# Kernel tuning notes

Measured on AMD Instinct MI355X. Metric: run time of the kernel, lower is better.

Reference implementation:

```python
import jax, jax.numpy as jnp
import numpy as np

H = 4       # N_head
C = 32      # c_hidden
CZ = 128    # c_z
N = 256
B = 1
EPS = 1e-5


def setup_inputs() -> dict:
    key = jax.random.key(0)
    ks = jax.random.split(key, 8)
    hc = H * C
    return {
        "z": jax.random.normal(ks[0], (B, N, N, CZ), dtype=jnp.float32),
        "ln_scale": jnp.ones((CZ,), dtype=jnp.float32),
        "ln_bias": jnp.zeros((CZ,), dtype=jnp.float32),
        "Wq": jax.random.normal(ks[1], (CZ, hc), dtype=jnp.float32) * 0.02,
        "Wk": jax.random.normal(ks[2], (CZ, hc), dtype=jnp.float32) * 0.02,
        "Wv": jax.random.normal(ks[3], (CZ, hc), dtype=jnp.float32) * 0.02,
        "Wb": jax.random.normal(ks[4], (CZ, H), dtype=jnp.float32) * 0.02,
        "Wg": jax.random.normal(ks[5], (CZ, hc), dtype=jnp.float32) * 0.02,
        "Wo": jax.random.normal(ks[6], (hc, CZ), dtype=jnp.float32) * 0.02,
    }


def reference(z, ln_scale, ln_bias, Wq, Wk, Wv, Wb, Wg, Wo):
    b, n = z.shape[0], z.shape[1]
    # LayerNorm over c_z
    mu = jnp.mean(z, axis=-1, keepdims=True)
    var = jnp.mean(jnp.square(z - mu), axis=-1, keepdims=True)
    zn = (z - mu) * jax.lax.rsqrt(var + EPS) * ln_scale + ln_bias
    # projections -> [B, N, N, H, C]
    q = (zn @ Wq).reshape(b, n, n, H, C)
    k = (zn @ Wk).reshape(b, n, n, H, C)
    v = (zn @ Wv).reshape(b, n, n, H, C)
    bias = zn @ Wb                                  # [B, N, N, H]
    g = jax.nn.sigmoid(zn @ Wg).reshape(b, n, n, H, C)
    # attention around starting node i: query at (i,j), keys/values at (i,k)
    scores = jnp.einsum('bijhd,bikhd->bijkh', q, k) * (1.0 / C ** 0.5)
    scores = scores + bias[:, None, :, :, :]        # bias[b, j, k, h]
    a = jax.nn.softmax(scores, axis=-2)             # softmax over k
    o = jnp.einsum('bijkh,bikhd->bijhd', a, v)      # [B, N, N, H, C]
    o = (g * o).reshape(b, n, n, H * C)
    return o @ Wo
```

## Files before the change

### kernel.cpp

```cpp
#include <hip/hip_runtime.h>
#include <math.h>

#define NN 256
#define CZ 128
#define NH 4
#define CH 32
#define HC 128
#define NPIX (NN*NN)
#define L2E   1.4426950408889634f
#define SCALE2 (0.17677669529663687f * 1.4426950408889634f)

typedef __attribute__((ext_vector_type(8))) short bf16x8;
typedef __attribute__((ext_vector_type(4))) float fx4;
typedef __attribute__((ext_vector_type(4))) unsigned u32x4;

__device__ __forceinline__ unsigned pack_hl(float x) {
    unsigned b  = __builtin_bit_cast(unsigned, x);
    unsigned hb = b & 0xFFFF0000u;
    float r = x - __builtin_bit_cast(float, hb);
    return hb | (__builtin_bit_cast(unsigned, r) >> 16);
}
__device__ __forceinline__ void load_split8(const float* p, bf16x8& h, bf16x8& l) {
    float4 x0 = *(const float4*)p;
    float4 x1 = *(const float4*)(p + 4);
    float xs[8] = {x0.x, x0.y, x0.z, x0.w, x1.x, x1.y, x1.z, x1.w};
    #pragma unroll
    for (int j = 0; j < 8; ++j) {
        unsigned b  = __builtin_bit_cast(unsigned, xs[j]);
        unsigned hb = b & 0xFFFF0000u;
        float r = xs[j] - __builtin_bit_cast(float, hb);
        h[j] = (short)(hb >> 16);
        l[j] = (short)(__builtin_bit_cast(unsigned, r) >> 16);
    }
}
__device__ __forceinline__ void deint8(const unsigned* p, bf16x8& h, bf16x8& l) {
    u32x4 e0 = *(const u32x4*)p;
    u32x4 e1 = *(const u32x4*)(p + 4);
    unsigned es[8] = {e0[0], e0[1], e0[2], e0[3], e1[0], e1[1], e1[2], e1[3]};
    unsigned hw[4], lw[4];
    #pragma unroll
    for (int j = 0; j < 4; ++j) {
        unsigned a = es[2 * j], b = es[2 * j + 1];
        hw[j] = (a >> 16) | (b & 0xFFFF0000u);
        lw[j] = (a & 0x0000FFFFu) | (b << 16);
    }
    h = __builtin_bit_cast(bf16x8, u32x4{hw[0], hw[1], hw[2], hw[3]});
    l = __builtin_bit_cast(bf16x8, u32x4{lw[0], lw[1], lw[2], lw[3]});
}

__global__ __launch_bounds__(256) void pack_w_kernel(
    const float* __restrict__ Wq, const float* __restrict__ Wk,
    const float* __restrict__ Wv, const float* __restrict__ Wg,
    const float* __restrict__ Wo, bf16x8* __restrict__ pk)
{
    int id  = blockIdx.x * 256 + threadIdx.x;
    int mid = id >> 11;
    int e   = id & 2047;
    const float* W = (mid == 0) ? Wq : (mid == 1) ? Wk : (mid == 2) ? Wv : (mid == 3) ? Wg : Wo;
    int quad = e & 3, n = (e >> 2) & 127, ks = e >> 9;
    int k0 = ks * 32 + quad * 8;
    bf16x8 h, l;
    #pragma unroll
    for (int j = 0; j < 8; ++j) {
        float x = W[(size_t)(k0 + j) * 128 + n];
        unsigned b  = __builtin_bit_cast(unsigned, x);
        unsigned hb = b & 0xFFFF0000u;
        float r = x - __builtin_bit_cast(float, hb);
        h[j] = (short)(hb >> 16);
        l[j] = (short)(__builtin_bit_cast(unsigned, r) >> 16);
    }
    pk[(size_t)mid * 4096 + e]        = h;
    pk[(size_t)mid * 4096 + 2048 + e] = l;
}

__global__ __launch_bounds__(256) void ln_proj_kernel(
    const float* __restrict__ z, const float* __restrict__ ls, const float* __restrict__ lb,
    const float* __restrict__ Wb, const bf16x8* __restrict__ pk,
    unsigned* __restrict__ q_pk, unsigned* __restrict__ k_pk, unsigned* __restrict__ v_pk,
    float* __restrict__ g_ws, float* __restrict__ bias_n)
{
    __shared__ float zsh[32][132];
    __shared__ float rsum[256], rsq[256];
    __shared__ float pmu[32], prs[32];

    const int t  = threadIdx.x;
    const int p0 = blockIdx.x * 32;
    const int i  = p0 >> 8;
    const int j0 = p0 & 255;

    const float4* z4 = (const float4*)(z + (size_t)p0 * CZ);
    #pragma unroll
    for (int r = 0; r < 4; ++r) {
        int idx4 = t + 256 * r;
        int p = idx4 >> 5, pos = idx4 & 31;
        *(float4*)&zsh[p][pos * 4] = z4[idx4];
    }
    __syncthreads();

    {
        int p = t >> 3, sg = t & 7;
        float s = 0.f, q = 0.f;
        #pragma unroll
        for (int u = 0; u < 16; ++u) { float x = zsh[p][sg * 16 + u]; s += x; q += x * x; }
        rsum[t] = s; rsq[t] = q;
    }
    __syncthreads();
    if (t < 32) {
        float s = 0.f, q = 0.f;
        #pragma unroll
        for (int g = 0; g < 8; ++g) { s += rsum[t * 8 + g]; q += rsq[t * 8 + g]; }
        float mu  = s * (1.0f / 128.0f);
        float var = q * (1.0f / 128.0f) - mu * mu;
        float a   = var + 1e-5f;
        float r   = rsqrtf(a);
        r = r * (1.5f - 0.5f * a * r * r);
        pmu[t] = mu; prs[t] = r;
    }
    __syncthreads();

    #pragma unroll
    for (int r4 = 0; r4 < 4; ++r4) {
        int idx4 = t + 256 * r4;
        int p = idx4 >> 5, pos = idx4 & 31;
        float4 v  = *(float4*)&zsh[p][pos * 4];
        float4 s4 = ((const float4*)ls)[pos];
        float4 b4 = ((const float4*)lb)[pos];
        float mu = pmu[p], rs = prs[p];
        v.x = (v.x - mu) * rs * s4.x + b4.x;
        v.y = (v.y - mu) * rs * s4.y + b4.y;
        v.z = (v.z - mu) * rs * s4.z + b4.z;
        v.w = (v.w - mu) * rs * s4.w + b4.w;
        *(float4*)&zsh[p][pos * 4] = v;
    }
    __syncthreads();

    const int wv = t >> 6, lane = t & 63;
    const int lrow = lane & 15, quad = lane >> 4;
    const bf16x8* ph = pk + (size_t)wv * 4096;
    const bf16x8* pl = ph + 2048;

    fx4 acc[2][8];
    #pragma unroll
    for (int mr = 0; mr < 2; ++mr)
        #pragma unroll
        for (int nc = 0; nc < 8; ++nc)
            acc[mr][nc] = fx4{0.f, 0.f, 0.f, 0.f};

    #pragma unroll
    for (int ks = 0; ks < 4; ++ks) {
        bf16x8 ah[2], al[2];
        #pragma unroll
        for (int mr = 0; mr < 2; ++mr)
            load_split8(&zsh[mr * 16 + lrow][ks * 32 + quad * 8], ah[mr], al[mr]);
        #pragma unroll
        for (int nc = 0; nc < 8; ++nc) {
            int bi = (ks * 128 + nc * 16 + lrow) * 4 + quad;
            bf16x8 bh = ph[bi], bl = pl[bi];
            #pragma unroll
            for (int mr = 0; mr < 2; ++mr) {
                acc[mr][nc] = __builtin_amdgcn_mfma_f32_16x16x32_bf16(ah[mr], bl, acc[mr][nc], 0, 0, 0);
                acc[mr][nc] = __builtin_amdgcn_mfma_f32_16x16x32_bf16(al[mr], bh, acc[mr][nc], 0, 0, 0);
                acc[mr][nc] = __builtin_amdgcn_mfma_f32_16x16x32_bf16(ah[mr], bh, acc[mr][nc], 0, 0, 0);
            }
        }
    }

    #pragma unroll
    for (int mr = 0; mr < 2; ++mr) {
        #pragma unroll
        for (int nc = 0; nc < 8; ++nc) {
            int cg = nc * 16 + lrow;
            int h = cg >> 5, cc = cg & 31;
            int jl = mr * 16 + quad * 4;
            fx4 a = acc[mr][nc];
            if (wv == 0) {
                unsigned* qp = q_pk + ((size_t)(i * NH + h) * NN + j0 + jl) * CH + cc;
                #pragma unroll
                for (int r = 0; r < 4; ++r) qp[r * CH] = pack_hl(a[r]);
            } else if (wv == 1) {
                unsigned* kp = k_pk + ((size_t)(i * NH + h) * NN + j0 + jl) * CH + cc;
                #pragma unroll
                for (int r = 0; r < 4; ++r) kp[r * CH] = pack_hl(a[r]);
            } else if (wv == 2) {
                u32x4 e = {pack_hl(a[0]), pack_hl(a[1]), pack_hl(a[2]), pack_hl(a[3])};
                *(u32x4*)(v_pk + ((size_t)(i * NH + h) * CH + cc) * NN + j0 + jl) = e;
            } else {
                float* gp = g_ws + (size_t)(p0 + jl) * HC + cg;
                #pragma unroll
                for (int r = 0; r < 4; ++r) gp[r * HC] = 1.0f / (1.0f + __expf(-a[r]));
            }
        }
    }

    if (t < 128) {
        int hh = t >> 5, p = t & 31;
        float b = 0.f;
        for (int d = 0; d < 128; ++d) b = fmaf(zsh[p][d], Wb[d * 4 + hh], b);
        bias_n[(size_t)hh * NPIX + (size_t)i * NN + j0 + p] = b * L2E;
    }
}

#define PSTR 40
__global__ __launch_bounds__(256) void attn_kernel(
    const unsigned* __restrict__ q_pk, const unsigned* __restrict__ k_pk,
    const unsigned* __restrict__ v_pk, const float* __restrict__ g_ws,
    const float* __restrict__ bias_n, float* __restrict__ go_ws)
{
    __shared__ unsigned short Psh[4][2][64 * PSTR];

    const int t = threadIdx.x;
    const int wv = t >> 6, lane = t & 63;
    const int lrow = lane & 15, quad = lane >> 4;
    const int h = blockIdx.x & 3, i = blockIdx.x >> 2;
    const int qb = wv * 64;

    const unsigned* qs = q_pk + (size_t)(i * NH + h) * NN * CH;
    const unsigned* ks = k_pk + (size_t)(i * NH + h) * NN * CH;
    const unsigned* vs = v_pk + (size_t)(i * NH + h) * CH * NN;
    const float*    bs = bias_n + (size_t)h * NPIX;

    bf16x8 qh[4], ql[4];
    #pragma unroll
    for (int nt = 0; nt < 4; ++nt)
        deint8(qs + (size_t)(qb + nt * 16 + lrow) * CH + quad * 8, qh[nt], ql[nt]);

    fx4 oacc[2][4];
    #pragma unroll
    for (int ct = 0; ct < 2; ++ct)
        #pragma unroll
        for (int nt = 0; nt < 4; ++nt)
            oacc[ct][nt] = fx4{0.f, 0.f, 0.f, 0.f};
    float lsum[4] = {0.f, 0.f, 0.f, 0.f};

    for (int kb = 0; kb < NN; kb += 32) {
        bf16x8 kh[2], kl_[2];
        #pragma unroll
        for (int mt = 0; mt < 2; ++mt)
            deint8(ks + (size_t)(kb + mt * 16 + lrow) * CH + quad * 8, kh[mt], kl_[mt]);
        bf16x8 vh[2], vl[2];
        #pragma unroll
        for (int ct = 0; ct < 2; ++ct)
            deint8(vs + (size_t)(ct * 16 + lrow) * NN + kb + quad * 8, vh[ct], vl[ct]);

        #pragma unroll
        for (int nt = 0; nt < 4; ++nt) {
            #pragma unroll
            for (int mt = 0; mt < 2; ++mt) {
                float4 bv = *(const float4*)(bs + (size_t)(qb + nt * 16 + lrow) * NN
                                                + kb + mt * 16 + quad * 4);

                fx4 sv = fx4{0.f, 0.f, 0.f, 0.f};
                sv = __builtin_amdgcn_mfma_f32_16x16x32_bf16(kh[mt], ql[nt], sv, 0, 0, 0);
                sv = __builtin_amdgcn_mfma_f32_16x16x32_bf16(kl_[mt], qh[nt], sv, 0, 0, 0);
                sv = __builtin_amdgcn_mfma_f32_16x16x32_bf16(kh[mt], qh[nt], sv, 0, 0, 0);

                float e0 = exp2f(fmaf(sv[0], SCALE2, bv.x));
                float e1 = exp2f(fmaf(sv[1], SCALE2, bv.y));
                float e2 = exp2f(fmaf(sv[2], SCALE2, bv.z));
                float e3 = exp2f(fmaf(sv[3], SCALE2, bv.w));
                lsum[nt] += (e0 + e1) + (e2 + e3);

                unsigned b0 = __builtin_bit_cast(unsigned, e0);
                unsigned b1 = __builtin_bit_cast(unsigned, e1);
                unsigned b2 = __builtin_bit_cast(unsigned, e2);
                unsigned b3 = __builtin_bit_cast(unsigned, e3);
                unsigned h01 = (b0 >> 16) | (b1 & 0xFFFF0000u);
                unsigned h23 = (b2 >> 16) | (b3 & 0xFFFF0000u);
                float r0 = e0 - __builtin_bit_cast(float, b0 & 0xFFFF0000u);
                float r1 = e1 - __builtin_bit_cast(float, b1 & 0xFFFF0000u);
                float r2 = e2 - __builtin_bit_cast(float, b2 & 0xFFFF0000u);
                float r3 = e3 - __builtin_bit_cast(float, b3 & 0xFFFF0000u);
                unsigned l01 = (__builtin_bit_cast(unsigned, r0) >> 16)
                             | (__builtin_bit_cast(unsigned, r1) & 0xFFFF0000u);
                unsigned l23 = (__builtin_bit_cast(unsigned, r2) >> 16)
                             | (__builtin_bit_cast(unsigned, r3) & 0xFFFF0000u);

                int wo = (nt * 16 + lrow) * PSTR + mt * 16 + quad * 4;
                *(uint2*)&Psh[wv][0][wo] = make_uint2(h01, h23);
                *(uint2*)&Psh[wv][1][wo] = make_uint2(l01, l23);
            }
        }

        #pragma unroll
        for (int nt = 0; nt < 4; ++nt) {
            bf16x8 pbh = *(const bf16x8*)&Psh[wv][0][(nt * 16 + lrow) * PSTR + quad * 8];
            bf16x8 pbl = *(const bf16x8*)&Psh[wv][1][(nt * 16 + lrow) * PSTR + quad * 8];
            #pragma unroll
            for (int ct = 0; ct < 2; ++ct) {
                oacc[ct][nt] = __builtin_amdgcn_mfma_f32_16x16x32_bf16(vh[ct], pbl, oacc[ct][nt], 0, 0, 0);
                oacc[ct][nt] = __builtin_amdgcn_mfma_f32_16x16x32_bf16(vl[ct], pbh, oacc[ct][nt], 0, 0, 0);
                oacc[ct][nt] = __builtin_amdgcn_mfma_f32_16x16x32_bf16(vh[ct], pbh, oacc[ct][nt], 0, 0, 0);
            }
        }
    }

    #pragma unroll
    for (int nt = 0; nt < 4; ++nt) {
        float s = lsum[nt];
        s += __shfl_xor(s, 16, 64);
        s += __shfl_xor(s, 32, 64);
        float inv = 1.0f / s;
        size_t pix = (size_t)i * NN + qb + nt * 16 + lrow;
        #pragma unroll
        for (int ct = 0; ct < 2; ++ct) {
            const float* gp = g_ws + pix * HC + h * CH + ct * 16 + quad * 4;
            float4 g4 = *(const float4*)gp;
            fx4 o = oacc[ct][nt];
            float4 r;
            r.x = g4.x * o[0] * inv;
            r.y = g4.y * o[1] * inv;
            r.z = g4.z * o[2] * inv;
            r.w = g4.w * o[3] * inv;
            *(float4*)(go_ws + pix * HC + h * CH + ct * 16 + quad * 4) = r;
        }
    }
}

__global__ __launch_bounds__(256) void outproj_kernel(
    const float* __restrict__ go_ws, const bf16x8* __restrict__ pk, float* __restrict__ out)
{
    __shared__ float gsh[64][132];
    const int t  = threadIdx.x;
    const int p0 = blockIdx.x * 64;

    const float4* g4 = (const float4*)(go_ws + (size_t)p0 * HC);
    #pragma unroll
    for (int r = 0; r < 8; ++r) {
        int idx4 = t + 256 * r;
        int p = idx4 >> 5, pos = idx4 & 31;
        *(float4*)&gsh[p][pos * 4] = g4[idx4];
    }
    __syncthreads();

    const int wv = t >> 6, lane = t & 63;
    const int lrow = lane & 15, quad = lane >> 4;
    const bf16x8* ph = pk + (size_t)4 * 4096;
    const bf16x8* pl = ph + 2048;

    fx4 acc[8];
    #pragma unroll
    for (int nc = 0; nc < 8; ++nc) acc[nc] = fx4{0.f, 0.f, 0.f, 0.f};

    #pragma unroll
    for (int ks = 0; ks < 4; ++ks) {
        bf16x8 ah, al;
        load_split8(&gsh[wv * 16 + lrow][ks * 32 + quad * 8], ah, al);
        #pragma unroll
        for (int nc = 0; nc < 8; ++nc) {
            int bi = (ks * 128 + nc * 16 + lrow) * 4 + quad;
            bf16x8 bh = ph[bi], bl = pl[bi];
            acc[nc] = __builtin_amdgcn_mfma_f32_16x16x32_bf16(ah, bl, acc[nc], 0, 0, 0);
            acc[nc] = __builtin_amdgcn_mfma_f32_16x16x32_bf16(al, bh, acc[nc], 0, 0, 0);
            acc[nc] = __builtin_amdgcn_mfma_f32_16x16x32_bf16(ah, bh, acc[nc], 0, 0, 0);
        }
    }

    #pragma unroll
    for (int nc = 0; nc < 8; ++nc) {
        #pragma unroll
        for (int r = 0; r < 4; ++r)
            out[(size_t)(p0 + wv * 16 + quad * 4 + r) * HC + nc * 16 + lrow] = acc[nc][r];
    }
}

extern "C" void kernel_launch(void* const* d_in, const int* in_sizes, int n_in,
                              void* d_out, int out_size, void* d_ws, size_t ws_size,
                              hipStream_t stream)
{
    const float* z  = (const float*)d_in[0];
    const float* ls = (const float*)d_in[1];
    const float* lb = (const float*)d_in[2];
    const float* Wq = (const float*)d_in[3];
    const float* Wk = (const float*)d_in[4];
    const float* Wv = (const float*)d_in[5];
    const float* Wb = (const float*)d_in[6];
    const float* Wg = (const float*)d_in[7];
    const float* Wo = (const float*)d_in[8];

    float* ws = (float*)d_ws;
    const size_t BIG = (size_t)NPIX * HC;
    unsigned* q_pk  = (unsigned*)ws;
    unsigned* k_pk  = (unsigned*)(ws + BIG);
    unsigned* v_pk  = (unsigned*)(ws + 2 * BIG);
    float* g_ws     = ws + 3 * BIG;
    float* go_ws    = ws + 4 * BIG;
    float* bias_n   = ws + 5 * BIG;
    bf16x8* pk      = (bf16x8*)(bias_n + (size_t)NH * NPIX);

    pack_w_kernel<<<40, 256, 0, stream>>>(Wq, Wk, Wv, Wg, Wo, pk);
    ln_proj_kernel<<<NPIX / 32, 256, 0, stream>>>(z, ls, lb, Wb, pk,
                                                  q_pk, k_pk, v_pk, g_ws, bias_n);
    attn_kernel<<<NN * NH, 256, 0, stream>>>(q_pk, k_pk, v_pk, g_ws, bias_n, go_ws);
    outproj_kernel<<<NPIX / 64, 256, 0, stream>>>(go_ws, pk, (float*)d_out);
}
```

Baseline: 247.4 us.

## Replace LDS round-trip of P tile with in-register permlane swaps

The attention kernel no longer writes the exponentiated score tile to shared memory and reads it back in the MFMA B-operand layout. It instead rearranges the packed bf16 hi/lo words across lanes with permlane32/permlane16 swap instructions, so the P·V MFMAs can consume them directly per query tile. It also wraps the MFMA groups in s_setprio and sets a launch-bounds occupancy hint. This removes the LDS traffic and its waits, but the swaps add VALU work and depend on the lane mapping being exactly right.

```diff
diff --git a/kernel.cpp b/kernel.cpp
--- a/kernel.cpp
+++ b/kernel.cpp
@@ -46,6 +46,22 @@
     }
     h = __builtin_bit_cast(bf16x8, u32x4{hw[0], hw[1], hw[2], hw[3]});
     l = __builtin_bit_cast(bf16x8, u32x4{lw[0], lw[1], lw[2], lw[3]});
+}
+
+__device__ __forceinline__ void qtrans(unsigned &x, unsigned &y) {
+#if __has_builtin(__builtin_amdgcn_permlane32_swap) && __has_builtin(__builtin_amdgcn_permlane16_swap)
+    {
+        auto r = __builtin_amdgcn_permlane32_swap(x, y, false, false);
+        x = r[0]; y = r[1];
+    }
+    {
+        auto r = __builtin_amdgcn_permlane16_swap(x, y, false, false);
+        x = r[0]; y = r[1];
+    }
+#else
+    asm("v_permlane32_swap_b32 %0, %1\n\t"
+        "v_permlane16_swap_b32 %0, %1" : "+v"(x), "+v"(y));
+#endif
 }
 
 __global__ __launch_bounds__(256) void pack_w_kernel(
@@ -200,14 +216,11 @@
     }
 }
 
-#define PSTR 40
-__global__ __launch_bounds__(256) void attn_kernel(
+__global__ __launch_bounds__(256, 4) void attn_kernel(
     const unsigned* __restrict__ q_pk, const unsigned* __restrict__ k_pk,
     const unsigned* __restrict__ v_pk, const float* __restrict__ g_ws,
     const float* __restrict__ bias_n, float* __restrict__ go_ws)
 {
-    __shared__ unsigned short Psh[4][2][64 * PSTR];
-
     const int t = threadIdx.x;
     const int wv = t >> 6, lane = t & 63;
     const int lrow = lane & 15, quad = lane >> 4;
@@ -244,15 +257,18 @@
 
         #pragma unroll
         for (int nt = 0; nt < 4; ++nt) {
+            unsigned w0h[2], w1h[2], w0l[2], w1l[2];
             #pragma unroll
             for (int mt = 0; mt < 2; ++mt) {
                 float4 bv = *(const float4*)(bs + (size_t)(qb + nt * 16 + lrow) * NN
                                                 + kb + mt * 16 + quad * 4);
 
                 fx4 sv = fx4{0.f, 0.f, 0.f, 0.f};
+                __builtin_amdgcn_s_setprio(1);
                 sv = __builtin_amdgcn_mfma_f32_16x16x32_bf16(kh[mt], ql[nt], sv, 0, 0, 0);
                 sv = __builtin_amdgcn_mfma_f32_16x16x32_bf16(kl_[mt], qh[nt], sv, 0, 0, 0);
                 sv = __builtin_amdgcn_mfma_f32_16x16x32_bf16(kh[mt], qh[nt], sv, 0, 0, 0);
+                __builtin_amdgcn_s_setprio(0);
 
                 float e0 = exp2f(fmaf(sv[0], SCALE2, bv.x));
                 float e1 = exp2f(fmaf(sv[1], SCALE2, bv.y));
@@ -274,23 +290,25 @@
                              | (__builtin_bit_cast(unsigned, r1) & 0xFFFF0000u);
                 unsigned l23 = (__builtin_bit_cast(unsigned, r2) >> 16)
                              | (__builtin_bit_cast(unsigned, r3) & 0xFFFF0000u);
-
-                int wo = (nt * 16 + lrow) * PSTR + mt * 16 + quad * 4;
-                *(uint2*)&Psh[wv][0][wo] = make_uint2(h01, h23);
-                *(uint2*)&Psh[wv][1][wo] = make_uint2(l01, l23);
+                w0h[mt] = h01; w1h[mt] = h23;
+                w0l[mt] = l01; w1l[mt] = l23;
             }
-        }
-
-        #pragma unroll
-        for (int nt = 0; nt < 4; ++nt) {
-            bf16x8 pbh = *(const bf16x8*)&Psh[wv][0][(nt * 16 + lrow) * PSTR + quad * 8];
-            bf16x8 pbl = *(const bf16x8*)&Psh[wv][1][(nt * 16 + lrow) * PSTR + quad * 8];
+
+            qtrans(w0h[0], w0h[1]);
+            qtrans(w1h[0], w1h[1]);
+            qtrans(w0l[0], w0l[1]);
+            qtrans(w1l[0], w1l[1]);
+            bf16x8 pbh = __builtin_bit_cast(bf16x8, u32x4{w0h[0], w1h[0], w0h[1], w1h[1]});
+            bf16x8 pbl = __builtin_bit_cast(bf16x8, u32x4{w0l[0], w1l[0], w0l[1], w1l[1]});
+
+            __builtin_amdgcn_s_setprio(1);
             #pragma unroll
             for (int ct = 0; ct < 2; ++ct) {
                 oacc[ct][nt] = __builtin_amdgcn_mfma_f32_16x16x32_bf16(vh[ct], pbl, oacc[ct][nt], 0, 0, 0);
                 oacc[ct][nt] = __builtin_amdgcn_mfma_f32_16x16x32_bf16(vl[ct], pbh, oacc[ct][nt], 0, 0, 0);
                 oacc[ct][nt] = __builtin_amdgcn_mfma_f32_16x16x32_bf16(vh[ct], pbh, oacc[ct][nt], 0, 0, 0);
             }
+            __builtin_amdgcn_s_setprio(0);
         }
     }
 
```

After: 272.0 us. 9.9% more time.
